# Kernel tuning notes

Measured on AMD Instinct MI355X. Metric: run time of the kernel, lower is better.

## Reference

```python
import jax, jax.numpy as jnp
import numpy as np


def setup_inputs() -> dict:
    key = jax.random.key(0)
    k1, k2, k3, k4 = jax.random.split(key, 4)
    B, C, H, W = 8, 64, 64, 64
    Ck = C // 8  # query/key channels
    x = jax.random.normal(k1, (B, C, H, W), dtype=jnp.float32)
    # 1x1 conv1d weights (bias=False); spectral norm only rescales the weight,
    # so plain matrices are math-equivalent at a given parameter value.
    wq = jax.random.normal(k2, (Ck, C), dtype=jnp.float32) * (1.0 / np.sqrt(C))
    wk = jax.random.normal(k3, (Ck, C), dtype=jnp.float32) * (1.0 / np.sqrt(C))
    wv = jax.random.normal(k4, (C, C), dtype=jnp.float32) * (1.0 / np.sqrt(C))
    gamma = jnp.array([0.5], dtype=jnp.float32)  # nonzero so attention path is exercised
    return {"x": x, "wq": wq, "wk": wk, "wv": wv, "gamma": gamma}


def reference(x, wq, wk, wv, gamma):
    B, C, H, W = x.shape
    xf = x.reshape(B, C, H * W)                      # [B, C, N]
    f = jnp.einsum('kc,bcn->bkn', wq, xf)            # [B, C/8, N]
    g = jnp.einsum('kc,bcn->bkn', wk, xf)            # [B, C/8, N]
    h = jnp.einsum('oc,bcn->bon', wv, xf)            # [B, C,   N]
    scores = jnp.einsum('bkn,bkm->bnm', f, g)        # f^T g, [B, N, N]
    beta = jax.nn.softmax(scores, axis=1)            # softmax over dim=1 (rows), as in torch
    o = jnp.einsum('bcn,bnm->bcm', h, beta)          # [B, C, N]
    out = gamma[0] * o + xf
    return out.reshape(B, C, H, W)
```

## Files before the change

### kernel.cpp

```cpp
#include <hip/hip_runtime.h>
#include <hip/hip_bf16.h>

typedef __bf16 bf16x8 __attribute__((ext_vector_type(8)));
typedef float f32x4 __attribute__((ext_vector_type(4)));
typedef float f32x16 __attribute__((ext_vector_type(16)));

#define MFMA16 __builtin_amdgcn_mfma_f32_16x16x32_bf16
#define MFMA32 __builtin_amdgcn_mfma_f32_32x32x16_bf16

__device__ __forceinline__ unsigned short f2b(float f) {
  unsigned int u = __float_as_uint(f);
  u += 0x7FFFu + ((u >> 16) & 1u);
  return (unsigned short)(u >> 16);
}

__device__ __forceinline__ float b2f(unsigned short s) {
  return __uint_as_float(((unsigned)s) << 16);
}

union U128 {
  uint4 u;
  unsigned short s[8];
  bf16x8 b;
};

union BPack {
  __hip_bfloat162 h2;
  unsigned u;
};

__device__ __forceinline__ unsigned packbf(float a, float b) {
  BPack p;
  p.h2 = __float22bfloat162_rn(make_float2(a, b));
  return p.u;
}

__global__ __launch_bounds__(256, 2) void proj_kernel(
    const float* __restrict__ x, const float* __restrict__ wq,
    const float* __restrict__ wk, const float* __restrict__ wv_w,
    unsigned short* __restrict__ f_t, unsigned short* __restrict__ g_t,
    unsigned short* __restrict__ h_out) {
  __shared__ unsigned short xT[64 * 64];
  __shared__ unsigned short wT[96 * 72];

  const int tid = (int)threadIdx.x;
  const int wvp = tid >> 6;
  const int lane = tid & 63;
  const int b = (int)blockIdx.x & 7;
  const int n0 = ((int)blockIdx.x >> 3) << 6;

  {
    const float* xb = x + ((size_t)b << 18) + n0 + lane;
    const int c0 = wvp * 16;
    float xv[16];
#pragma unroll
    for (int cc = 0; cc < 16; ++cc) xv[cc] = xb[(size_t)(c0 + cc) << 12];
#pragma unroll
    for (int p = 0; p < 4; ++p) {
      const int c = c0 + 4 * p;
      uint2 d;
      d.x = packbf(xv[4 * p + 0], xv[4 * p + 1]);
      d.y = packbf(xv[4 * p + 2], xv[4 * p + 3]);
      const int g = c >> 3;
      const int idx = lane * 64 + (((g ^ (lane & 7)) << 3) | (((c >> 2) & 1) << 2));
      *(uint2*)&xT[idx] = d;
    }
  }
#pragma unroll
  for (int i = 0; i < 20; ++i) {
    const int idx = i * 256 + tid;
    const float wval = (idx < 512) ? wq[idx] * 1.44269504f
                     : (idx < 1024) ? wk[idx - 512]
                                    : wv_w[idx - 1024];
    wT[(idx >> 6) * 72 + (idx & 63)] = f2b(wval);
  }
  __syncthreads();

  const int t = lane & 15, q = lane >> 4;
  const int nloc = wvp * 16 + t;
  U128 Bf[2];
#pragma unroll
  for (int kp = 0; kp < 2; ++kp) {
    const int g = kp * 4 + q;
    Bf[kp].u = *(const uint4*)&xT[nloc * 64 + ((g ^ (nloc & 7)) << 3)];
  }
  const int nabs = n0 + nloc;
#pragma unroll
  for (int rt = 0; rt < 5; ++rt) {
    f32x4 acc = {0.f, 0.f, 0.f, 0.f};
#pragma unroll
    for (int kp = 0; kp < 2; ++kp) {
      U128 Af;
      Af.u = *(const uint4*)&wT[(rt * 16 + t) * 72 + ((kp * 4 + q) << 3)];
      acc = MFMA16(Af.b, Bf[kp].b, acc, 0, 0, 0);
    }
#pragma unroll
    for (int reg = 0; reg < 4; ++reg) {
      const int r = rt * 16 + 4 * q + reg;
      const unsigned short v = f2b(acc[reg]);
      if (r < 8)
        f_t[((size_t)((b << 12) + nabs) << 3) + r] = v;
      else if (r < 16)
        g_t[((size_t)((b << 12) + nabs) << 3) + (r - 8)] = v;
      else
        h_out[((size_t)b << 18) + ((size_t)(nabs >> 3) << 9) +
              ((r - 16) << 3) + (nabs & 7)] = v;
    }
  }
}

__global__ __launch_bounds__(256, 4) void attn_kernel(
    const unsigned short* __restrict__ f_t, const unsigned short* __restrict__ g_t,
    const unsigned short* __restrict__ h, const float* __restrict__ x,
    const float* __restrict__ gamma, float* __restrict__ out) {
  __shared__ unsigned short Opart[4][32][66];
  __shared__ float lred[4][32];
  __shared__ float lsum[32];

  const int tid = (int)threadIdx.x;
  const int wave = tid >> 6;
  const int lane = tid & 63;
  const int ml = lane & 31;
  const int hh = lane >> 5;

  const int b = (int)blockIdx.x & 7;
  const int m32 = ((int)blockIdx.x >> 3) << 5;

  const unsigned short* fb = f_t + ((size_t)b << 15);
  const unsigned short* hb = h + ((size_t)b << 18);

  U128 G;
  G.u = make_uint4(0u, 0u, 0u, 0u);
  if (hh == 0) G.u = *(const uint4*)(g_t + ((size_t)((b << 12) + m32 + ml) << 3));

  f32x16 O0 = {}, O1 = {};
  float lpa = 0.f, lpb = 0.f;

  const int nbase = wave << 10;

  const unsigned short* fp = fb + ((size_t)(nbase + ml) << 3);
  const unsigned short* hp = hb + ((nbase >> 3) << 9) + (hh << 9) + (ml << 3);

  U128 F, Fn, Ha[4], Hn[4];
  F.u = *(const uint4*)(fp);
  Ha[0].u = *(const uint4*)(hp);
  Ha[1].u = *(const uint4*)(hp + 256);
  Ha[2].u = *(const uint4*)(hp + 1024);
  Ha[3].u = *(const uint4*)(hp + 1024 + 256);

  for (int it = 0; it < 32; ++it) {
    const int adv = (it < 31) ? 1 : 0;
    Fn.u = *(const uint4*)(fp + adv * 256);
    const unsigned short* hq = hp + adv * 2048;
    Hn[0].u = *(const uint4*)(hq);
    Hn[1].u = *(const uint4*)(hq + 256);
    Hn[2].u = *(const uint4*)(hq + 1024);
    Hn[3].u = *(const uint4*)(hq + 1024 + 256);
    fp += 256;
    hp += 2048;

    const f32x16 z = {};
    f32x16 S = MFMA32(F.b, G.b, z, 0, 0, 0);

    float e[16];
#pragma unroll
    for (int r = 0; r < 16; ++r) e[r] = __builtin_amdgcn_exp2f(S[r]);
#pragma unroll
    for (int r = 0; r < 8; ++r) {
      lpa += e[2 * r];
      lpb += e[2 * r + 1];
    }

#pragma unroll
    for (int kt = 0; kt < 2; ++kt) {
      const unsigned A0 = packbf(e[8 * kt + 0], e[8 * kt + 1]);
      const unsigned A1 = packbf(e[8 * kt + 2], e[8 * kt + 3]);
      const unsigned B0 = packbf(e[8 * kt + 4], e[8 * kt + 5]);
      const unsigned B1 = packbf(e[8 * kt + 6], e[8 * kt + 7]);
      const unsigned s0 = hh ? A0 : B0;
      const unsigned s1 = hh ? A1 : B1;
      const unsigned r0 = (unsigned)__shfl_xor((int)s0, 32, 64);
      const unsigned r1 = (unsigned)__shfl_xor((int)s1, 32, 64);
      U128 P;
      P.u.x = hh ? r0 : A0;
      P.u.y = hh ? r1 : A1;
      P.u.z = hh ? B0 : r0;
      P.u.w = hh ? B1 : r1;
      if (kt == 0) {
        O0 = MFMA32(Ha[0].b, P.b, O0, 0, 0, 0);
        O1 = MFMA32(Ha[1].b, P.b, O1, 0, 0, 0);
      } else {
        O0 = MFMA32(Ha[2].b, P.b, O0, 0, 0, 0);
        O1 = MFMA32(Ha[3].b, P.b, O1, 0, 0, 0);
      }
    }

    F = Fn;
#pragma unroll
    for (int k = 0; k < 4; ++k) Ha[k] = Hn[k];
  }

  float lp = lpa + lpb;
  lp += __shfl_xor(lp, 32, 64);
  if (hh == 0) lred[wave][ml] = lp;
#pragma unroll
  for (int r = 0; r < 8; ++r) {
    const int c0 = ((2 * r) & 3) + 8 * (r >> 1) + 4 * hh;
    *(unsigned*)&Opart[wave][ml][c0] = packbf(O0[2 * r], O0[2 * r + 1]);
    *(unsigned*)&Opart[wave][ml][c0 + 32] = packbf(O1[2 * r], O1[2 * r + 1]);
  }
  __syncthreads();
  if (tid < 32)
    lsum[tid] = (lred[0][tid] + lred[1][tid]) + (lred[2][tid] + lred[3][tid]);
  __syncthreads();

  const int c = tid >> 2;
  const int m0l = (tid & 3) << 3;
  const float gam = gamma[0];
  float a[8];
#pragma unroll
  for (int j = 0; j < 8; ++j) a[j] = 0.f;
#pragma unroll
  for (int w = 0; w < 4; ++w)
#pragma unroll
    for (int j = 0; j < 8; ++j) a[j] += b2f(Opart[w][m0l + j][c]);

  const f32x4 l0 = *(const f32x4*)&lsum[m0l];
  const f32x4 l1 = *(const f32x4*)&lsum[m0l + 4];
  const size_t oi = (((size_t)b * 64 + c) << 12) + m32 + m0l;
  f32x4 xo0 = *(const f32x4*)(x + oi);
  f32x4 xo1 = *(const f32x4*)(x + oi + 4);
#pragma unroll
  for (int j = 0; j < 4; ++j) {
    xo0[j] += gam / l0[j] * a[j];
    xo1[j] += gam / l1[j] * a[j + 4];
  }
  *(f32x4*)(out + oi) = xo0;
  *(f32x4*)(out + oi + 4) = xo1;
}

extern "C" void kernel_launch(void* const* d_in, const int* in_sizes, int n_in,
                              void* d_out, int out_size, void* d_ws, size_t ws_size,
                              hipStream_t stream) {
  (void)in_sizes; (void)n_in; (void)out_size; (void)ws_size;
  const float* x = (const float*)d_in[0];
  const float* wq = (const float*)d_in[1];
  const float* wk = (const float*)d_in[2];
  const float* wv = (const float*)d_in[3];
  const float* gamma = (const float*)d_in[4];
  float* out = (float*)d_out;

  unsigned short* f_t = (unsigned short*)d_ws;
  unsigned short* g_t = f_t + (size_t)8 * 4096 * 8;
  unsigned short* h = g_t + (size_t)8 * 4096 * 8;

  proj_kernel<<<512, 256, 0, stream>>>(x, wq, wk, wv, f_t, g_t, h);
  attn_kernel<<<1024, 256, 0, stream>>>(f_t, g_t, h, x, gamma, out);
}
```

Measured before the change: 108.4 us.

## Use 512-thread attention blocks covering 64 columns and software-pipeline the score MFMA

```diff
diff --git a/kernel.cpp b/kernel.cpp
--- a/kernel.cpp
+++ b/kernel.cpp
@@ -109,22 +109,25 @@
   }
 }
 
-__global__ __launch_bounds__(256, 4) void attn_kernel(
+__global__ __launch_bounds__(512, 4) void attn_kernel(
     const unsigned short* __restrict__ f_t, const unsigned short* __restrict__ g_t,
     const unsigned short* __restrict__ h, const float* __restrict__ x,
     const float* __restrict__ gamma, float* __restrict__ out) {
-  __shared__ unsigned short Opart[4][32][66];
-  __shared__ float lred[4][32];
-  __shared__ float lsum[32];
+  __shared__ unsigned short Opart[8][32][66];
+  __shared__ float lred[8][32];
+  __shared__ float lsum[2][32];
 
   const int tid = (int)threadIdx.x;
   const int wave = tid >> 6;
   const int lane = tid & 63;
   const int ml = lane & 31;
   const int hh = lane >> 5;
+  const int nq = wave & 3;
+  const int mh = wave >> 2;
 
   const int b = (int)blockIdx.x & 7;
-  const int m32 = ((int)blockIdx.x >> 3) << 5;
+  const int m64 = ((int)blockIdx.x >> 3) << 6;
+  const int m32 = m64 + mh * 32;
 
   const unsigned short* fb = f_t + ((size_t)b << 15);
   const unsigned short* hb = h + ((size_t)b << 18);
@@ -136,31 +139,31 @@
   f32x16 O0 = {}, O1 = {};
   float lpa = 0.f, lpb = 0.f;
 
-  const int nbase = wave << 10;
+  const int nbase = nq << 10;
 
   const unsigned short* fp = fb + ((size_t)(nbase + ml) << 3);
   const unsigned short* hp = hb + ((nbase >> 3) << 9) + (hh << 9) + (ml << 3);
 
-  U128 F, Fn, Ha[4], Hn[4];
-  F.u = *(const uint4*)(fp);
-  Ha[0].u = *(const uint4*)(hp);
-  Ha[1].u = *(const uint4*)(hp + 256);
-  Ha[2].u = *(const uint4*)(hp + 1024);
-  Ha[3].u = *(const uint4*)(hp + 1024 + 256);
+  U128 F1;
+  F1.u = *(const uint4*)(fp);
+  const f32x16 z = {};
+  f32x16 S = MFMA32(F1.b, G.b, z, 0, 0, 0);
+  F1.u = *(const uint4*)(fp + 256);
 
   for (int it = 0; it < 32; ++it) {
-    const int adv = (it < 31) ? 1 : 0;
-    Fn.u = *(const uint4*)(fp + adv * 256);
-    const unsigned short* hq = hp + adv * 2048;
-    Hn[0].u = *(const uint4*)(hq);
-    Hn[1].u = *(const uint4*)(hq + 256);
-    Hn[2].u = *(const uint4*)(hq + 1024);
-    Hn[3].u = *(const uint4*)(hq + 1024 + 256);
+    U128 Ha0, Ha1, Ha2, Ha3;
+    Ha0.u = *(const uint4*)(hp);
+    Ha1.u = *(const uint4*)(hp + 256);
+    Ha2.u = *(const uint4*)(hp + 1024);
+    Ha3.u = *(const uint4*)(hp + 1024 + 256);
+    hp += 2048;
+
+    U128 Fn;
+    Fn.u = *(const uint4*)(fp + 512);
     fp += 256;
-    hp += 2048;
-
-    const f32x16 z = {};
-    f32x16 S = MFMA32(F.b, G.b, z, 0, 0, 0);
+
+    f32x16 Snext = MFMA32(F1.b, G.b, z, 0, 0, 0);
+    F1 = Fn;
 
     float e[16];
 #pragma unroll
@@ -187,17 +190,15 @@
       P.u.z = hh ? B0 : r0;
       P.u.w = hh ? B1 : r1;
       if (kt == 0) {
-        O0 = MFMA32(Ha[0].b, P.b, O0, 0, 0, 0);
-        O1 = MFMA32(Ha[1].b, P.b, O1, 0, 0, 0);
+        O0 = MFMA32(Ha0.b, P.b, O0, 0, 0, 0);
+        O1 = MFMA32(Ha1.b, P.b, O1, 0, 0, 0);
       } else {
-        O0 = MFMA32(Ha[2].b, P.b, O0, 0, 0, 0);
-        O1 = MFMA32(Ha[3].b, P.b, O1, 0, 0, 0);
+        O0 = MFMA32(Ha2.b, P.b, O0, 0, 0, 0);
+        O1 = MFMA32(Ha3.b, P.b, O1, 0, 0, 0);
       }
     }
 
-    F = Fn;
-#pragma unroll
-    for (int k = 0; k < 4; ++k) Ha[k] = Hn[k];
+    S = Snext;
   }
 
   float lp = lpa + lpb;
@@ -210,12 +211,19 @@
     *(unsigned*)&Opart[wave][ml][c0 + 32] = packbf(O1[2 * r], O1[2 * r + 1]);
   }
   __syncthreads();
-  if (tid < 32)
-    lsum[tid] = (lred[0][tid] + lred[1][tid]) + (lred[2][tid] + lred[3][tid]);
+  if (tid < 64) {
+    const int half = tid >> 5, mm = tid & 31;
+    const int w0 = half << 2;
+    lsum[half][mm] = (lred[w0][mm] + lred[w0 + 1][mm]) +
+                     (lred[w0 + 2][mm] + lred[w0 + 3][mm]);
+  }
   __syncthreads();
 
-  const int c = tid >> 2;
-  const int m0l = (tid & 3) << 3;
+  const int half = tid >> 8;
+  const int t = tid & 255;
+  const int c = t >> 2;
+  const int m0l = (t & 3) << 3;
+  const int w0 = half << 2;
   const float gam = gamma[0];
   float a[8];
 #pragma unroll
@@ -223,11 +231,11 @@
 #pragma unroll
   for (int w = 0; w < 4; ++w)
 #pragma unroll
-    for (int j = 0; j < 8; ++j) a[j] += b2f(Opart[w][m0l + j][c]);
-
-  const f32x4 l0 = *(const f32x4*)&lsum[m0l];
-  const f32x4 l1 = *(const f32x4*)&lsum[m0l + 4];
-  const size_t oi = (((size_t)b * 64 + c) << 12) + m32 + m0l;
+    for (int j = 0; j < 8; ++j) a[j] += b2f(Opart[w0 + w][m0l + j][c]);
+
+  const f32x4 l0 = *(const f32x4*)&lsum[half][m0l];
+  const f32x4 l1 = *(const f32x4*)&lsum[half][m0l + 4];
+  const size_t oi = (((size_t)b * 64 + c) << 12) + m64 + half * 32 + m0l;
   f32x4 xo0 = *(const f32x4*)(x + oi);
   f32x4 xo1 = *(const f32x4*)(x + oi + 4);
 #pragma unroll
@@ -255,5 +263,5 @@
   unsigned short* h = g_t + (size_t)8 * 4096 * 8;
 
   proj_kernel<<<512, 256, 0, stream>>>(x, wq, wk, wv, f_t, g_t, h);
-  attn_kernel<<<1024, 256, 0, stream>>>(f_t, g_t, h, x, gamma, out);
-}
+  attn_kernel<<<512, 512, 0, stream>>>(f_t, g_t, h, x, gamma, out);
+}
```

Result: slower. 111.0 us (+2.4%).
